# Kernel optimization log

Measured on AMD Instinct MI355X. Metric: run time of the kernel, lower is better.

## Reference

```python
import jax, jax.numpy as jnp
import numpy as np

D = 1024   # cfg.hid (downscaled from 8192)
M = 20000  # cfg.mem_c // 2 (downscaled)
B, LQ = 4, 8
PLAST_S = 0.05
IMPORTANCE = 1.0


def mha_shared_kv(q, kv_k, kv_v, Wi, bi, Wo, bo, nheads):
    """torch nn.MultiheadAttention (batch_first) with batch-shared K/V.
    q: [B,Lq,D]; kv_k/kv_v: [Lk,D] shared across batch (avoids the .repeat()
    materialization in the original torch code while computing identical math)."""
    dh = D // nheads
    Wq, Wk, Wv = jnp.split(Wi, 3, axis=0)
    bq, bk, bv = jnp.split(bi, 3)
    qp = (jnp.einsum('bqd,ed->bqe', q, Wq) + bq) * (dh ** -0.5)
    kp = kv_k @ Wk.T + bk              # [Lk,D]
    vp = kv_v @ Wv.T + bv              # [Lk,D]
    qh = qp.reshape(q.shape[0], q.shape[1], nheads, dh)      # [B,Lq,h,dh]
    kh = kp.reshape(kp.shape[0], nheads, dh)                 # [Lk,h,dh]
    vh = vp.reshape(vp.shape[0], nheads, dh)                 # [Lk,h,dh]
    scores = jnp.einsum('bqhd,khd->bhqk', qh, kh)            # [B,h,Lq,Lk]
    attn = jax.nn.softmax(scores, axis=-1)
    ctx = jnp.einsum('bhqk,khd->bqhd', attn, vh)
    ctx = ctx.reshape(q.shape[0], q.shape[1], D)
    return ctx @ Wo.T + bo


def setup_inputs() -> dict:
    key = jax.random.key(0)
    ks = jax.random.split(key, 16)
    s = 0.02
    return {
        'q':    jax.random.normal(ks[0], (B, LQ, D), jnp.float32),
        'data': jax.random.normal(ks[1], (B, D), jnp.float32),
        'ek':   jax.random.normal(ks[2], (M, D), jnp.float32),
        'ev':   jax.random.normal(ks[3], (M, D), jnp.float32),
        'sk':   jax.random.normal(ks[4], (M, D), jnp.float32),
        'sv':   jax.random.normal(ks[5], (M, D), jnp.float32),
        'wm':   jax.random.normal(ks[6], (10, D), jnp.float32),
        'Wi_e': jax.random.normal(ks[7], (3 * D, D), jnp.float32) * s,
        'bi_e': jnp.zeros((3 * D,), jnp.float32),
        'Wo_e': jax.random.normal(ks[8], (D, D), jnp.float32) * s,
        'bo_e': jnp.zeros((D,), jnp.float32),
        'Wi_s': jax.random.normal(ks[9], (3 * D, D), jnp.float32) * s,
        'bi_s': jnp.zeros((3 * D,), jnp.float32),
        'Wo_s': jax.random.normal(ks[10], (D, D), jnp.float32) * s,
        'bo_s': jnp.zeros((D,), jnp.float32),
        'Wi_w': jax.random.normal(ks[11], (3 * D, D), jnp.float32) * s,
        'bi_w': jnp.zeros((3 * D,), jnp.float32),
        'Wo_w': jax.random.normal(ks[12], (D, D), jnp.float32) * s,
        'bo_w': jnp.zeros((D,), jnp.float32),
        'Wrp':  jax.random.normal(ks[13], (D, 3 * D), jnp.float32) * s,
        'brp':  jnp.zeros((D,), jnp.float32),
        'eu':   jnp.zeros((M,), jnp.float32),
    }


def reference(q, data, ek, ev, sk, sv, wm,
              Wi_e, bi_e, Wo_e, bo_e,
              Wi_s, bi_s, Wo_s, bo_s,
              Wi_w, bi_w, Wo_w, bo_w,
              Wrp, brp, eu):
    # ---- NeuroMemory.read ----
    e_r = mha_shared_kv(q, ek, ev, Wi_e, bi_e, Wo_e, bo_e, 16)
    s_r = mha_shared_kv(q, sk, sv, Wi_s, bi_s, Wo_s, bo_s, 16)
    w_r = mha_shared_kv(q, wm, wm, Wi_w, bi_w, Wo_w, bo_w, 8)
    read_out = jnp.concatenate([e_r, s_r, w_r], axis=-1) @ Wrp.T + brp  # [B,Lq,D]

    # ---- NeuroMemory.write (episodic, Hebbian plasticity update) ----
    scores = data @ ek.T                       # [B,M]
    probs = jax.nn.softmax(scores, axis=-1)    # [B,M]
    upd = probs * (PLAST_S * IMPORTANCE)       # [B,M]
    u = upd.mean(axis=0)[:, None]              # [M,1] (batch-mean update strength)
    d = data.mean(axis=0)[None, :]             # [1,D]
    new_ek = ek * (1.0 - u) + d * u            # [M,D]
    new_ev = ev * (1.0 - u) + d * u            # [M,D]
    new_eu = eu * 0.99 + jax.lax.stop_gradient(probs.sum(axis=0))  # [M]
    return (read_out, new_ek, new_ev, new_eu)
```

## Files before the change

kernel.cpp:

```cpp
#include <hip/hip_runtime.h>
#include <hip/hip_fp16.h>
#include <hip/hip_bf16.h>
#include <cstdint>
#include <cstddef>

#define D_HID 1024
#define MEM_M 20000
#define NBATCH 4
#define BL 32
#define NROWS 512
#define SROWS_E 516
#define SROWS_S 512
#define BK 32
#define LDT 40
#define PV_NC 8

typedef __attribute__((ext_vector_type(8))) short short8;
typedef __attribute__((ext_vector_type(4))) float f32x4;
typedef __attribute__((ext_vector_type(16))) float f32x16;
typedef __attribute__((ext_vector_type(4))) unsigned short us4;

__device__ inline ushort f2bf(float f) {
    __hip_bfloat16 b = __float2bfloat16(f);
    return *reinterpret_cast<ushort*>(&b);
}
__device__ inline float h2f(ushort u) {
    __half h; *reinterpret_cast<ushort*>(&h) = u; return __half2float(h);
}

__device__ __forceinline__ void block_sync_lds() {
    asm volatile("s_waitcnt lgkmcnt(0)" ::: "memory");
    __builtin_amdgcn_s_barrier();
}

struct SkDesc  { const float* A; const float* B; int K; int M; };
struct SkDescs { SkDesc d[5]; };
struct RdDesc  { const float* bias; float* dst; int M; int ldc; float alpha; };
struct RdDescs { RdDesc d[5]; };

__device__ __forceinline__ void skinny_body(const SkDesc dd, float* __restrict__ part,
                                            int gk, int k0, int n0, int tid)
{
    __shared__ float As[32][132];
    __shared__ float Bs[64][129];
    const int K = dd.K, M = dd.M;
    {
        const int r = tid >> 3, cbl = (tid & 7) * 16;
        if (r < M) {
            const float* src = dd.A + (size_t)r * K + k0 + cbl;
            #pragma unroll
            for (int i = 0; i < 4; ++i) {
                const float4 v = *(const float4*)(src + i * 4);
                As[r][cbl + i * 4 + 0] = v.x; As[r][cbl + i * 4 + 1] = v.y;
                As[r][cbl + i * 4 + 2] = v.z; As[r][cbl + i * 4 + 3] = v.w;
            }
        } else {
            #pragma unroll
            for (int i = 0; i < 16; ++i) As[r][cbl + i] = 0.f;
        }
    }
    {
        const int r = tid >> 2, cbl = (tid & 3) * 32;
        const float* src = dd.B + (size_t)(n0 + r) * K + k0 + cbl;
        #pragma unroll
        for (int i = 0; i < 8; ++i) {
            const float4 v = *(const float4*)(src + i * 4);
            Bs[r][cbl + i * 4 + 0] = v.x; Bs[r][cbl + i * 4 + 1] = v.y;
            Bs[r][cbl + i * 4 + 2] = v.z; Bs[r][cbl + i * 4 + 3] = v.w;
        }
    }
    __syncthreads();
    const int n = tid & 63, mg = tid >> 6;
    float acc[8];
    #pragma unroll
    for (int i = 0; i < 8; ++i) acc[i] = 0.f;
    #pragma unroll 4
    for (int k = 0; k < 128; k += 4) {
        const float b0 = Bs[n][k + 0], b1 = Bs[n][k + 1];
        const float b2 = Bs[n][k + 2], b3 = Bs[n][k + 3];
        #pragma unroll
        for (int i = 0; i < 8; ++i) {
            const float4 a = *(const float4*)&As[mg * 8 + i][k];
            acc[i] = fmaf(a.x, b0, fmaf(a.y, b1, fmaf(a.z, b2, fmaf(a.w, b3, acc[i]))));
        }
    }
    #pragma unroll
    for (int i = 0; i < 8; ++i)
        part[((size_t)gk * 32 + mg * 8 + i) * 1024 + n0 + n] = acc[i];
}

__global__ __launch_bounds__(256)
void k_skinny(SkDescs ds, float* __restrict__ part)
{
    skinny_body(ds.d[blockIdx.z], part,
                blockIdx.z * gridDim.y + blockIdx.y,
                blockIdx.y * 128, blockIdx.x * 64, threadIdx.x);
}

__global__ __launch_bounds__(256)
void k_head(SkDescs ds, float* __restrict__ part,
            const float* __restrict__ ek, const float* __restrict__ sk,
            ushort* __restrict__ kvb)
{
    const int bx = blockIdx.x;
    const int tid = threadIdx.x;
    if (bx < 640) {
        const int g = bx >> 7;
        const int rem = bx & 127;
        const int kc = rem >> 4;
        const int n0 = (rem & 15) * 64;
        skinny_body(ds.d[g], part, g * 8 + kc, kc * 128, n0, tid);
    } else {
        const size_t nchunks = (size_t)2 * MEM_M * D_HID / 8;
        for (size_t i = (size_t)(bx - 640) * 256 + tid; i < nchunks;
             i += (size_t)1408 * 256) {
            const size_t base = i * 8;
            const float* src = (base < (size_t)MEM_M * D_HID)
                             ? (ek + base) : (sk + base - (size_t)MEM_M * D_HID);
            const float4 v0 = *(const float4*)(src);
            const float4 v1 = *(const float4*)(src + 4);
            alignas(16) ushort o[8];
            o[0] = f2bf(v0.x); o[1] = f2bf(v0.y); o[2] = f2bf(v0.z); o[3] = f2bf(v0.w);
            o[4] = f2bf(v1.x); o[5] = f2bf(v1.y); o[6] = f2bf(v1.z); o[7] = f2bf(v1.w);
            *(short8*)(kvb + base) = *(const short8*)o;
        }
    }
}

__global__ __launch_bounds__(256)
void k_skred(RdDescs ds, const float* __restrict__ part, int nkc)
{
    const int g = blockIdx.y;
    const int m = blockIdx.x;
    const RdDesc dd = ds.d[g];
    if (m >= dd.M) return;
    const int c = threadIdx.x * 4;
    float4 s = make_float4(0.f, 0.f, 0.f, 0.f);
    for (int kc = 0; kc < nkc; ++kc) {
        const float4 v = *(const float4*)&part[((size_t)(g * nkc + kc) * 32 + m) * 1024 + c];
        s.x += v.x; s.y += v.y; s.z += v.z; s.w += v.w;
    }
    const float4 b = *(const float4*)(dd.bias + c);
    float4 o;
    o.x = (s.x + b.x) * dd.alpha; o.y = (s.y + b.y) * dd.alpha;
    o.z = (s.z + b.z) * dd.alpha; o.w = (s.w + b.w) * dd.alpha;
    *(float4*)(dd.dst + (size_t)m * dd.ldc + c) = o;
}

__global__ __launch_bounds__(256)
void mfma_scores(const ushort* __restrict__ A_e, const ushort* __restrict__ ekb,
                 const ushort* __restrict__ A_s, const ushort* __restrict__ skb,
                 __half* __restrict__ S_e, __half* __restrict__ S_s,
                 __half* __restrict__ swr,
                 const float* __restrict__ c0_e, const float* __restrict__ c0_s)
{
    __shared__ ushort As[2][128][LDT];
    __shared__ ushort Bs[2][128][LDT];
    const int tid = threadIdx.x;
    const int i = blockIdx.x + 9 * blockIdx.y;
    const int xcd = i & 7, idx = i >> 3;
    const int wg = (xcd < 5 ? xcd * 177 : 885 + (xcd - 5) * 176) + idx;
    const int mi = wg % 9, nbk = wg / 9;
    const int bank = (mi >= 5);
    const int m0 = (bank ? (mi - 5) : mi) * 128;
    const int n0 = nbk * 128;
    const ushort* __restrict__ A = bank ? A_s : A_e;
    const ushort* __restrict__ B = bank ? skb : ekb;
    const float* __restrict__ c0 = bank ? c0_s : c0_e;
    const int Mreal = bank ? SROWS_S : SROWS_E;

    const int wid = tid >> 6, lane = tid & 63;
    const int wr = (wid >> 1) * 64, wc = (wid & 1) * 64;
    const int l31 = lane & 31, l2 = lane >> 5;

    const int srow = tid >> 1;
    const int ac = (tid & 1) * 16;
    int gbrow = n0 + srow; if (gbrow > MEM_M - 1) gbrow = MEM_M - 1;
    const ushort* Ap = A + (size_t)(m0 + srow) * 1024 + ac;
    const ushort* Bp = B + (size_t)gbrow * 1024 + ac;

    f32x16 acc[2][2];
    #pragma unroll
    for (int fm = 0; fm < 2; ++fm)
        #pragma unroll
        for (int fn = 0; fn < 2; ++fn)
            #pragma unroll
            for (int r = 0; r < 16; ++r) acc[fm][fn][r] = 0.f;

    auto MF = [&](int bu) {
        short8 a[2][2], b[2][2];
        #pragma unroll
        for (int f = 0; f < 2; ++f)
            #pragma unroll
            for (int kh = 0; kh < 2; ++kh) {
                a[f][kh] = *(const short8*)&As[bu][wr + f * 32 + l31][kh * 16 + l2 * 8];
                b[f][kh] = *(const short8*)&Bs[bu][wc + f * 32 + l31][kh * 16 + l2 * 8];
            }
        #pragma unroll
        for (int fm = 0; fm < 2; ++fm)
            #pragma unroll
            for (int fn = 0; fn < 2; ++fn)
                #pragma unroll
                for (int kh = 0; kh < 2; ++kh)
                    acc[fm][fn] = __builtin_amdgcn_mfma_f32_32x32x16_bf16(
                        a[fm][kh], b[fn][kh], acc[fm][fn], 0, 0, 0);
    };

    short8 a00, a01, b00, b01;
    short8 a10, a11, b10, b11;

#define SC_LOAD0(KT) { a00 = *(const short8*)(Ap + (KT)); a01 = *(const short8*)(Ap + (KT) + 8); \
                       b00 = *(const short8*)(Bp + (KT)); b01 = *(const short8*)(Bp + (KT) + 8); }
#define SC_LOAD1(KT) { a10 = *(const short8*)(Ap + (KT)); a11 = *(const short8*)(Ap + (KT) + 8); \
                       b10 = *(const short8*)(Bp + (KT)); b11 = *(const short8*)(Bp + (KT) + 8); }
#define SC_STORE0(BU) { *(short8*)&As[BU][srow][ac] = a00; *(short8*)&As[BU][srow][ac + 8] = a01; \
                        *(short8*)&Bs[BU][srow][ac] = b00; *(short8*)&Bs[BU][srow][ac + 8] = b01; }
#define SC_STORE1(BU) { *(short8*)&As[BU][srow][ac] = a10; *(short8*)&As[BU][srow][ac + 8] = a11; \
                        *(short8*)&Bs[BU][srow][ac] = b10; *(short8*)&Bs[BU][srow][ac + 8] = b11; }

    SC_LOAD0(0);
    SC_LOAD1(32);
    SC_STORE0(0);
    block_sync_lds();
    for (int it = 0; it < 16; ++it) {
        const int kt = it * 64;
        if (it < 15) SC_LOAD0(kt + 64);
        MF(0);
        SC_STORE1(1);
        block_sync_lds();
        if (it < 15) SC_LOAD1(kt + 96);
        MF(1);
        if (it < 15) SC_STORE0(0);
        block_sync_lds();
    }
#undef SC_LOAD0
#undef SC_LOAD1
#undef SC_STORE0
#undef SC_STORE1

    #pragma unroll
    for (int fm = 0; fm < 2; ++fm) {
        #pragma unroll
        for (int fn = 0; fn < 2; ++fn) {
            #pragma unroll
            for (int r = 0; r < 16; ++r) {
                const int row = m0 + wr + fm * 32 + (r & 3) + 8 * (r >> 2) + 4 * l2;
                if (row >= Mreal) continue;
                const int col = n0 + wc + fn * 32 + l31;
                if (col >= MEM_M) continue;
                const __half hv = __float2half(acc[fm][fn][r] + c0[row]);
                if (bank) S_s[(size_t)row * MEM_M + col] = hv;
                else if (row < NROWS) S_e[(size_t)row * MEM_M + col] = hv;
                else swr[(size_t)(row - NROWS) * MEM_M + col] = hv;
            }
        }
    }
}

__global__ __launch_bounds__(256)
void mfma_pv(const ushort* __restrict__ P_e, const ushort* __restrict__ P_s,
             const ushort* __restrict__ evb, const ushort* __restrict__ svb,
             float* __restrict__ part)
{
    __shared__ ushort As[2][128][LDT];
    __shared__ ushort Bs[2][128][LDT];
    const int tid = threadIdx.x;
    const int bid = blockIdx.x + 8 * (blockIdx.y + 4 * blockIdx.z);
    const int wgs = (bid & 7) * 64 + (bid >> 3);
    const int nI = wgs & 7, mI = (wgs >> 3) & 3;
    const int z = wgs >> 5;
    const int bank = z >> 3, c = z & 7;
    const ushort* __restrict__ P = bank ? P_s : P_e;
    const ushort* __restrict__ Vb = bank ? svb : evb;
    const int m0 = mI * 128, n0 = nI * 128;
    const int ks0 = (c * 625) / PV_NC, ks1 = ((c + 1) * 625) / PV_NC;
    const int wid = tid >> 6, lane = tid & 63;
    const int wr = (wid >> 1) * 64, wc = (wid & 1) * 64;
    const int l31 = lane & 31, l2 = lane >> 5;
    const int kb = (tid & 7) * 4, nb2 = (tid >> 3) * 4;
    const int srow = tid >> 1, ac = (tid & 1) * 16;
    const ushort* Pp = P + (size_t)(m0 + srow) * MEM_M + ac;

    f32x16 acc[2][2];
    #pragma unroll
    for (int fm = 0; fm < 2; ++fm)
        #pragma unroll
        for (int fn = 0; fn < 2; ++fn)
            #pragma unroll
            for (int r = 0; r < 16; ++r) acc[fm][fn][r] = 0.f;

    auto MF = [&](int bu) {
        short8 a[2][2], b[2][2];
        #pragma unroll
        for (int f = 0; f < 2; ++f)
            #pragma unroll
            for (int kh = 0; kh < 2; ++kh) {
                a[f][kh] = *(const short8*)&As[bu][wr + f * 32 + l31][kh * 16 + l2 * 8];
                b[f][kh] = *(const short8*)&Bs[bu][wc + f * 32 + l31][kh * 16 + l2 * 8];
            }
        #pragma unroll
        for (int fm = 0; fm < 2; ++fm)
            #pragma unroll
            for (int fn = 0; fn < 2; ++fn)
                #pragma unroll
                for (int kh = 0; kh < 2; ++kh)
                    acc[fm][fn] = __builtin_amdgcn_mfma_f32_32x32x16_bf16(
                        a[fm][kh], b[fn][kh], acc[fm][fn], 0, 0, 0);
    };

    short8 pa00, pa01, pa10, pa11;
    us4 q0[4], q1[4];

#define PV_LOAD0(T) { const int kt = (T) * 32; \
    pa00 = *(const short8*)(Pp + kt); pa01 = *(const short8*)(Pp + kt + 8); \
    q0[0] = *(const us4*)(Vb + (size_t)(kt + kb + 0) * 1024 + n0 + nb2); \
    q0[1] = *(const us4*)(Vb + (size_t)(kt + kb + 1) * 1024 + n0 + nb2); \
    q0[2] = *(const us4*)(Vb + (size_t)(kt + kb + 2) * 1024 + n0 + nb2); \
    q0[3] = *(const us4*)(Vb + (size_t)(kt + kb + 3) * 1024 + n0 + nb2); }
#define PV_LOAD1(T) { const int kt = (T) * 32; \
    pa10 = *(const short8*)(Pp + kt); pa11 = *(const short8*)(Pp + kt + 8); \
    q1[0] = *(const us4*)(Vb + (size_t)(kt + kb + 0) * 1024 + n0 + nb2); \
    q1[1] = *(const us4*)(Vb + (size_t)(kt + kb + 1) * 1024 + n0 + nb2); \
    q1[2] = *(const us4*)(Vb + (size_t)(kt + kb + 2) * 1024 + n0 + nb2); \
    q1[3] = *(const us4*)(Vb + (size_t)(kt + kb + 3) * 1024 + n0 + nb2); }
#define PV_STORE0(BU) { \
    *(short8*)&As[BU][srow][ac] = pa00; *(short8*)&As[BU][srow][ac + 8] = pa01; \
    us4 w; \
    w.x = q0[0].x; w.y = q0[1].x; w.z = q0[2].x; w.w = q0[3].x; \
    *(us4*)&Bs[BU][nb2 + 0][kb] = w; \
    w.x = q0[0].y; w.y = q0[1].y; w.z = q0[2].y; w.w = q0[3].y; \
    *(us4*)&Bs[BU][nb2 + 1][kb] = w; \
    w.x = q0[0].z; w.y = q0[1].z; w.z = q0[2].z; w.w = q0[3].z; \
    *(us4*)&Bs[BU][nb2 + 2][kb] = w; \
    w.x = q0[0].w; w.y = q0[1].w; w.z = q0[2].w; w.w = q0[3].w; \
    *(us4*)&Bs[BU][nb2 + 3][kb] = w; }
#define PV_STORE1(BU) { \
    *(short8*)&As[BU][srow][ac] = pa10; *(short8*)&As[BU][srow][ac + 8] = pa11; \
    us4 w; \
    w.x = q1[0].x; w.y = q1[1].x; w.z = q1[2].x; w.w = q1[3].x; \
    *(us4*)&Bs[BU][nb2 + 0][kb] = w; \
    w.x = q1[0].y; w.y = q1[1].y; w.z = q1[2].y; w.w = q1[3].y; \
    *(us4*)&Bs[BU][nb2 + 1][kb] = w; \
    w.x = q1[0].z; w.y = q1[1].z; w.z = q1[2].z; w.w = q1[3].z; \
    *(us4*)&Bs[BU][nb2 + 2][kb] = w; \
    w.x = q1[0].w; w.y = q1[1].w; w.z = q1[2].w; w.w = q1[3].w; \
    *(us4*)&Bs[BU][nb2 + 3][kb] = w; }

    PV_LOAD0(ks0);
    if (ks0 + 1 < ks1) PV_LOAD1(ks0 + 1);
    PV_STORE0(0);
    block_sync_lds();
    for (int t = ks0; t < ks1; t += 2) {
        if (t + 2 < ks1) PV_LOAD0(t + 2);
        MF(0);
        if (t + 1 < ks1) PV_STORE1(1);
        block_sync_lds();
        if (t + 1 < ks1) {
            if (t + 3 < ks1) PV_LOAD1(t + 3);
            MF(1);
            if (t + 2 < ks1) PV_STORE0(0);
            block_sync_lds();
        }
    }
#undef PV_LOAD0
#undef PV_LOAD1
#undef PV_STORE0
#undef PV_STORE1

    float* __restrict__ po = part + (size_t)z * NROWS * 1024;
    #pragma unroll
    for (int fm = 0; fm < 2; ++fm)
        #pragma unroll
        for (int fn = 0; fn < 2; ++fn)
            #pragma unroll
            for (int r = 0; r < 16; ++r) {
                const int row = m0 + wr + fm * 32 + (r & 3) + 8 * (r >> 2) + 4 * l2;
                const int col = n0 + wc + fn * 32 + l31;
                po[(size_t)row * 1024 + col] = acc[fm][fn][r];
            }
}

__global__ __launch_bounds__(256)
void k_T(const float* __restrict__ qp,
         const float* __restrict__ Wi_e, const float* __restrict__ bi_e,
         const float* __restrict__ Wi_s, const float* __restrict__ bi_s,
         ushort* __restrict__ A_e, float* __restrict__ c0_e,
         ushort* __restrict__ A_s, float* __restrict__ c0_s,
         const float* __restrict__ data, float* __restrict__ dmean)
{
    const int bq = blockIdx.x;
    const int tid = threadIdx.x;
    if (bq >= 128) {
        if (bq < 252) {
            const int row = SROWS_E + (bq - 128);
            us4 z4; z4.x = 0; z4.y = 0; z4.z = 0; z4.w = 0;
            *(us4*)(A_e + (size_t)row * 1024 + tid * 4) = z4;
        } else {
            for (int t = tid; t < D_HID; t += 256) {
                float s = 0.f;
                #pragma unroll
                for (int b = 0; b < NBATCH; ++b) s += data[b * D_HID + t];
                dmean[t] = 0.25f * s;
                #pragma unroll
                for (int b = 0; b < NBATCH; ++b)
                    A_e[(size_t)(NROWS + b) * 1024 + t] = f2bf(data[b * D_HID + t]);
            }
            if (tid < NBATCH) c0_e[NROWS + tid] = 0.f;
        }
        return;
    }
    const int bank = bq >> 6;
    const int h = (bq >> 2) & 15;
    const int q4 = bq & 3;
    const float* qpB = qp + (size_t)bank * BL * D_HID;
    const float* Wk = (bank ? Wi_s : Wi_e) + (size_t)D_HID * D_HID;
    const float* bk = (bank ? bi_s : bi_e) + D_HID;
    ushort* T  = bank ? A_s : A_e;
    float* c0 = bank ? c0_s : c0_e;

    __shared__ float qs[32][64];
    for (int i = tid; i < 32 * 64; i += 256) {
        const int r = i >> 6, j = i & 63;
        qs[r][j] = qpB[(size_t)r * D_HID + h * 64 + j];
    }
    __syncthreads();
    const int e = q4 * 256 + tid;
    float acc[32];
    #pragma unroll
    for (int r = 0; r < 32; ++r) acc[r] = 0.f;
    for (int j = 0; j < 64; ++j) {
        const float w = Wk[(size_t)(h * 64 + j) * D_HID + e];
        #pragma unroll
        for (int r = 0; r < 32; ++r) acc[r] = fmaf(qs[r][j], w, acc[r]);
    }
    #pragma unroll
    for (int r = 0; r < 32; ++r) T[(size_t)(r * 16 + h) * 1024 + e] = f2bf(acc[r]);
    if (q4 == 0 && tid < 32) {
        float s = 0.f;
        for (int j = 0; j < 64; ++j) s += qs[tid][j] * bk[h * 64 + j];
        c0[tid * 16 + h] = s;
    }
}

__global__ __launch_bounds__(256)
void k_softmax(__half* __restrict__ S_e, __half* __restrict__ S_s,
               __half* __restrict__ swr,
               float* __restrict__ mrow, float* __restrict__ lrow,
               const float* __restrict__ ev, const float* __restrict__ sv,
               ushort* __restrict__ evb, ushort* __restrict__ svb)
{
    const int bx = blockIdx.x;
    const int tid = threadIdx.x;
    if (bx >= SROWS_E + SROWS_S) {
        const size_t nchunks = (size_t)2 * MEM_M * D_HID / 8;
        for (size_t i = (size_t)(bx - (SROWS_E + SROWS_S)) * 256 + tid; i < nchunks;
             i += (size_t)1408 * 256) {
            const size_t base = i * 8;
            const bool second = base >= (size_t)MEM_M * D_HID;
            const float* src = second ? (sv + base - (size_t)MEM_M * D_HID) : (ev + base);
            ushort* dst = second ? (svb + base - (size_t)MEM_M * D_HID) : (evb + base);
            const float4 v0 = *(const float4*)(src);
            const float4 v1 = *(const float4*)(src + 4);
            alignas(16) ushort o[8];
            o[0] = f2bf(v0.x); o[1] = f2bf(v0.y); o[2] = f2bf(v0.z); o[3] = f2bf(v0.w);
            o[4] = f2bf(v1.x); o[5] = f2bf(v1.y); o[6] = f2bf(v1.z); o[7] = f2bf(v1.w);
            *(short8*)dst = *(const short8*)o;
        }
        return;
    }
    const int row = bx;
    ushort* p; bool conv = true;
    if (row < NROWS) p = (ushort*)(S_e + (size_t)row * MEM_M);
    else if (row < SROWS_E) { p = (ushort*)(swr + (size_t)(row - NROWS) * MEM_M); conv = false; }
    else p = (ushort*)(S_s + (size_t)(row - SROWS_E) * MEM_M);
    __shared__ float red_m[256];
    __shared__ float red_l[256];
    float m = -3.0e38f, l = 0.f;
    for (int c = tid; c < MEM_M / 8; c += 256) {
        alignas(16) ushort t[8];
        *(short8*)t = *(const short8*)(p + c * 8);
        float v[8];
        #pragma unroll
        for (int j = 0; j < 8; ++j) v[j] = h2f(t[j]);
        float cm = v[0];
        #pragma unroll
        for (int j = 1; j < 8; ++j) cm = fmaxf(cm, v[j]);
        const float nm = fmaxf(m, cm);
        float s = 0.f;
        #pragma unroll
        for (int j = 0; j < 8; ++j) s += __expf(v[j] - nm);
        l = l * __expf(m - nm) + s;
        m = nm;
    }
    red_m[tid] = m; red_l[tid] = l; __syncthreads();
    for (int s = 128; s > 0; s >>= 1) {
        if (tid < s) {
            const float m2 = fmaxf(red_m[tid], red_m[tid + s]);
            red_l[tid] = red_l[tid] * __expf(red_m[tid] - m2)
                       + red_l[tid + s] * __expf(red_m[tid + s] - m2);
            red_m[tid] = m2;
        }
        __syncthreads();
    }
    const float rm = red_m[0];
    if (conv) {
        for (int c = tid; c < MEM_M / 8; c += 256) {
            alignas(16) ushort t[8];
            *(short8*)t = *(const short8*)(p + c * 8);
            alignas(16) ushort o[8];
            #pragma unroll
            for (int j = 0; j < 8; ++j) o[j] = f2bf(__expf(h2f(t[j]) - rm));
            *(short8*)(p + c * 8) = *(const short8*)o;
        }
    }
    if (tid == 0) { mrow[row] = rm; lrow[row] = red_l[0]; }
}

__global__ __launch_bounds__(256)
void k_uk(const __half* __restrict__ swr,
          const float* __restrict__ mrow, const float* __restrict__ lrow,
          const float* __restrict__ eu,
          float* __restrict__ u, float* __restrict__ out_eu)
{
    const int k = blockIdx.x * 256 + threadIdx.x;
    if (k >= MEM_M) return;
    float sp = 0.f;
    #pragma unroll
    for (int b = 0; b < NBATCH; ++b) {
        const int row = NROWS + b;
        sp += __expf(__half2float(swr[(size_t)b * MEM_M + k]) - mrow[row]) / lrow[row];
    }
    u[k] = 0.05f * 0.25f * sp;
    out_eu[k] = eu[k] * 0.99f + sp;
}

__global__ __launch_bounds__(256)
void k_pvred_upd(const float* __restrict__ part, const float* __restrict__ lrow,
                 float* __restrict__ R,
                 const float* __restrict__ ev, const float* __restrict__ u,
                 const float* __restrict__ dmean, float* __restrict__ out_ev)
{
    const int tid = threadIdx.x;
    if (blockIdx.x < 1024) {
        const size_t perb4 = (size_t)NROWS * 1024 / 4;
        const size_t i = (size_t)blockIdx.x * 256 + tid;
        const int bank = i >= perb4;
        const size_t off4 = i - (size_t)bank * perb4;
        const int m = (int)(off4 >> 8);
        const float inv = 1.f / lrow[bank ? (SROWS_E + m) : m];
        const float4* p = (const float4*)part + (size_t)bank * PV_NC * perb4 + off4;
        float4 s = make_float4(0.f, 0.f, 0.f, 0.f);
        #pragma unroll
        for (int c = 0; c < PV_NC; ++c) {
            const float4 v = p[(size_t)c * perb4];
            s.x += v.x; s.y += v.y; s.z += v.z; s.w += v.w;
        }
        s.x *= inv; s.y *= inv; s.z *= inv; s.w *= inv;
        ((float4*)R)[i] = s;
    } else {
        const int bid = blockIdx.x - 1024;
        const size_t n4 = (size_t)MEM_M * D_HID / 4;
        for (size_t i = (size_t)bid * 256 + tid; i < n4; i += (size_t)1024 * 256) {
            const int k = (int)(i >> 8);
            const int c = (int)(i & 255);
            const float uk = u[k];
            const float om = 1.f - uk;
            const float4 dd = ((const float4*)dmean)[c];
            const float4 b = ((const float4*)ev)[i];
            float4 ob;
            ob.x = b.x * om + dd.x * uk; ob.y = b.y * om + dd.y * uk;
            ob.z = b.z * om + dd.z * uk; ob.w = b.w * om + dd.w * uk;
            ((float4*)out_ev)[i] = ob;
        }
    }
}

__global__ __launch_bounds__(256)
void k_tail(const float* __restrict__ R,
            const float* __restrict__ Wi_e, const float* __restrict__ bi_e,
            const float* __restrict__ Wi_s, const float* __restrict__ bi_s,
            float* __restrict__ ctx,
            const float* __restrict__ qp, const float* __restrict__ kpw,
            const float* __restrict__ vpw,
            const float* __restrict__ ek, const float* __restrict__ u,
            const float* __restrict__ dmean, float* __restrict__ out_ek)
{
    __shared__ float sm[12384];
    const int tid = threadIdx.x;
    const int bx = blockIdx.x;
    if (bx < 32) {
        const int bank = bx >> 4;
        const int h = bx & 15;
        const float* Rb = R + (size_t)bank * NROWS * D_HID;
        const float* Wv = (bank ? Wi_s : Wi_e) + (size_t)2 * D_HID * D_HID;
        const float* bv = (bank ? bi_s : bi_e) + 2 * D_HID;
        float* cb = ctx + (size_t)bank * BL * D_HID;
        float (*Rs)[129] = (float(*)[129])sm;
        float (*Ws)[129] = (float(*)[129])(sm + 32 * 129);
        const int j = tid & 63;
        const int g = tid >> 6;
        float acc[8];
        #pragma unroll
        for (int i = 0; i < 8; ++i) acc[i] = 0.f;
        for (int ec = 0; ec < D_HID; ec += 128) {
            for (int i = tid; i < 32 * 128; i += 256) {
                const int r = i >> 7, e = i & 127;
                Rs[r][e] = Rb[(size_t)(r * 16 + h) * D_HID + ec + e];
            }
            for (int i = tid; i < 64 * 128; i += 256) {
                const int r = i >> 7, e = i & 127;
                Ws[r][e] = Wv[(size_t)(h * 64 + r) * D_HID + ec + e];
            }
            __syncthreads();
            for (int e = 0; e < 128; ++e) {
                const float w = Ws[j][e];
                #pragma unroll
                for (int i = 0; i < 8; ++i)
                    acc[i] = fmaf(Rs[g + 4 * i][e], w, acc[i]);
            }
            __syncthreads();
        }
        #pragma unroll
        for (int i = 0; i < 8; ++i) {
            const int bl = g + 4 * i;
            cb[(size_t)bl * D_HID + h * 64 + j] = acc[i] + bv[h * 64 + j];
        }
    } else if (bx < 64) {
        const int bl = bx - 32;
        float* q = sm;
        float (*kp)[1024] = (float(*)[1024])(sm + 1024);
        float (*pp)[10] = (float(*)[10])(sm + 1024 + 10240);
        const float* qrow = qp + (size_t)(2 * BL + bl) * D_HID;
        for (int i = tid; i < D_HID; i += 256) q[i] = qrow[i];
        for (int i = tid; i < 10 * D_HID; i += 256) kp[i >> 10][i & 1023] = kpw[i];
        __syncthreads();
        if (tid < 80) {
            const int h = tid / 10, k = tid % 10;
            float s = 0.f;
            for (int jj = 0; jj < 128; ++jj) s += q[h * 128 + jj] * kp[k][h * 128 + jj];
            pp[h][k] = s;
        }
        __syncthreads();
        if (tid < 8) {
            float m = -3.0e38f;
            for (int k = 0; k < 10; ++k) m = fmaxf(m, pp[tid][k]);
            float e[10]; float l = 0.f;
            for (int k = 0; k < 10; ++k) { e[k] = __expf(pp[tid][k] - m); l += e[k]; }
            const float inv = 1.f / l;
            for (int k = 0; k < 10; ++k) pp[tid][k] = e[k] * inv;
        }
        __syncthreads();
        float* cw = ctx + (size_t)(2 * BL + bl) * D_HID;
        for (int f = tid; f < D_HID; f += 256) {
            const int h = f >> 7;
            float s = 0.f;
            #pragma unroll
            for (int k = 0; k < 10; ++k) s += pp[h][k] * vpw[(size_t)k * D_HID + f];
            cw[f] = s;
        }
    } else {
        const int bid = bx - 64;
        const size_t n4 = (size_t)MEM_M * D_HID / 4;
        for (size_t i = (size_t)bid * 256 + tid; i < n4; i += (size_t)1024 * 256) {
            const int k = (int)(i >> 8);
            const int c = (int)(i & 255);
            const float uk = u[k];
            const float om = 1.f - uk;
            const float4 dd = ((const float4*)dmean)[c];
            const float4 a = ((const float4*)ek)[i];
            float4 oa;
            oa.x = a.x * om + dd.x * uk; oa.y = a.y * om + dd.y * uk;
            oa.z = a.z * om + dd.z * uk; oa.w = a.w * om + dd.w * uk;
            ((float4*)out_ek)[i] = oa;
        }
    }
}

extern "C" void kernel_launch(void* const* d_in, const int* in_sizes, int n_in,
                              void* d_out, int out_size, void* d_ws, size_t ws_size,
                              hipStream_t stream)
{
    (void)in_sizes; (void)n_in; (void)out_size; (void)ws_size;
    const float* q    = (const float*)d_in[0];
    const float* data = (const float*)d_in[1];
    const float* ek   = (const float*)d_in[2];
    const float* ev   = (const float*)d_in[3];
    const float* sk   = (const float*)d_in[4];
    const float* sv   = (const float*)d_in[5];
    const float* wm   = (const float*)d_in[6];
    const float* Wi_e = (const float*)d_in[7];
    const float* bi_e = (const float*)d_in[8];
    const float* Wo_e = (const float*)d_in[9];
    const float* bo_e = (const float*)d_in[10];
    const float* Wi_s = (const float*)d_in[11];
    const float* bi_s = (const float*)d_in[12];
    const float* Wo_s = (const float*)d_in[13];
    const float* bo_s = (const float*)d_in[14];
    const float* Wi_w = (const float*)d_in[15];
    const float* bi_w = (const float*)d_in[16];
    const float* Wo_w = (const float*)d_in[17];
    const float* bo_w = (const float*)d_in[18];
    const float* Wrp  = (const float*)d_in[19];
    const float* brp  = (const float*)d_in[20];
    const float* eu   = (const float*)d_in[21];

    float* out = (float*)d_out;
    float* out_read = out;
    float* out_ek = out + 32768;
    float* out_ev = out_ek + 20480000;
    float* out_eu = out_ev + 20480000;

    float* ws    = (float*)d_ws;
    float* qp    = ws;
    float* A_e   = qp + 98304;
    float* A_s   = A_e + 655360;
    float* c0_e  = A_s + 524288;
    float* c0_s  = c0_e + 640;
    float* dmean = c0_s + 512;
    float* u     = dmean + 1024;
    float* mrow  = u + 20480;
    float* lrow  = mrow + 1032;
    float* kpw   = lrow + 1032;
    float* vpw   = kpw + 10240;
    float* ctx   = vpw + 10240;
    float* cat   = ctx + 98304;
    float* skpart = cat + 98304;
    float* Rbuf  = skpart;
    __half* swr  = (__half*)(skpart + 1310720);

    ushort* A_e16 = (ushort*)A_e;
    ushort* A_s16 = (ushort*)A_s;

    ushort* ekb = (ushort*)out_ek;
    ushort* skb = ekb + (size_t)MEM_M * D_HID;
    ushort* evb = (ushort*)out_ek;
    float* part = out_ek + 10240000;
    __half* S_e = (__half*)out_ev;
    __half* S_s = S_e + (size_t)NROWS * MEM_M;
    ushort* svb = (ushort*)(S_s + (size_t)NROWS * MEM_M);

    const dim3 b256(256);
    const float sc16 = 0.125f;
    const float sc8  = 0.08838834764831845f;

    SkDescs s1;
    s1.d[0] = {q,  Wi_e,            1024, 32};
    s1.d[1] = {q,  Wi_s,            1024, 32};
    s1.d[2] = {q,  Wi_w,            1024, 32};
    s1.d[3] = {wm, Wi_w + 1048576,  1024, 10};
    s1.d[4] = {wm, Wi_w + 2097152,  1024, 10};
    k_head<<<2048, b256, 0, stream>>>(s1, skpart, ek, sk, ekb);
    RdDescs r1;
    r1.d[0] = {bi_e,        qp,         32, 1024, sc16};
    r1.d[1] = {bi_s,        qp + 32768, 32, 1024, sc16};
    r1.d[2] = {bi_w,        qp + 65536, 32, 1024, sc8};
    r1.d[3] = {bi_w + 1024, kpw,        10, 1024, 1.f};
    r1.d[4] = {bi_w + 2048, vpw,        10, 1024, 1.f};
    k_skred<<<dim3(32, 5), b256, 0, stream>>>(r1, skpart, 8);

    k_T<<<253, b256, 0, stream>>>(qp, Wi_e, bi_e, Wi_s, bi_s,
                                  A_e16, c0_e, A_s16, c0_s, data, dmean);

    mfma_scores<<<dim3(9, 157), b256, 0, stream>>>(A_e16, ekb, A_s16, skb,
                                                   S_e, S_s, swr, c0_e, c0_s);

    k_softmax<<<SROWS_E + SROWS_S + 1408, b256, 0, stream>>>(
        S_e, S_s, swr, mrow, lrow, ev, sv, evb, svb);
    k_uk<<<79, b256, 0, stream>>>(swr, mrow, lrow, eu, u, out_eu);

    mfma_pv<<<dim3(8, 4, 2 * PV_NC), b256, 0, stream>>>(
        (const ushort*)S_e, (const ushort*)S_s, evb, svb, part);

    k_pvred_upd<<<2048, b256, 0, stream>>>(part, lrow, Rbuf, ev, u, dmean, out_ev);

    k_tail<<<1088, b256, 0, stream>>>(Rbuf, Wi_e, bi_e, Wi_s, bi_s, ctx,
                                      qp, kpw, vpw, ek, u, dmean, out_ek);

    SkDescs s2;
    s2.d[0] = {ctx,         Wo_e, 1024, 32};
    s2.d[1] = {ctx + 32768, Wo_s, 1024, 32};
    s2.d[2] = {ctx + 65536, Wo_w, 1024, 32};
    s2.d[3] = {ctx,         Wo_e, 1024, 32};
    s2.d[4] = {ctx,         Wo_e, 1024, 32};
    k_skinny<<<dim3(16, 8, 3), b256, 0, stream>>>(s2, skpart);
    RdDescs r2;
    r2.d[0] = {bo_e, cat,        32, 3072, 1.f};
    r2.d[1] = {bo_s, cat + 1024, 32, 3072, 1.f};
    r2.d[2] = {bo_w, cat + 2048, 32, 3072, 1.f};
    r2.d[3] = r2.d[0];
    r2.d[4] = r2.d[0];
    k_skred<<<dim3(32, 3), b256, 0, stream>>>(r2, skpart, 8);

    SkDescs s3;
    s3.d[0] = {cat, Wrp, 3072, 32};
    s3.d[1] = s3.d[0]; s3.d[2] = s3.d[0]; s3.d[3] = s3.d[0]; s3.d[4] = s3.d[0];
    k_skinny<<<dim3(16, 24, 1), b256, 0, stream>>>(s3, skpart);
    RdDescs r3;
    r3.d[0] = {brp, out_read, 32, 1024, 1.f};
    r3.d[1] = r3.d[0]; r3.d[2] = r3.d[0]; r3.d[3] = r3.d[0]; r3.d[4] = r3.d[0];
    k_skred<<<dim3(32, 1), b256, 0, stream>>>(r3, skpart, 24);
}
```

Baseline: 497.8 us.

## Fuse exp and row-sum into score GEMM epilogue, drop max-subtraction softmax pass

The score GEMM epilogue now writes exp(score) as bf16 straight into the P buffers and accumulates per-row sums with a warp shuffle reduction plus atomicAdd. This removes the separate softmax kernel that re-read and rewrote the full fp16 score matrices. Only the four write-path rows still get a small max/sum stats kernel, and the ev/sv bf16 conversion moves into k_uk. The trade-off is that the row max is no longer subtracted, so numerical safety rests on scores being small enough not to overflow exp. Row-sum atomics also make the summation order nondeterministic.

```diff
diff --git a/kernel.cpp b/kernel.cpp
--- a/kernel.cpp
+++ b/kernel.cpp
@@ -150,9 +150,10 @@
 __global__ __launch_bounds__(256)
 void mfma_scores(const ushort* __restrict__ A_e, const ushort* __restrict__ ekb,
                  const ushort* __restrict__ A_s, const ushort* __restrict__ skb,
-                 __half* __restrict__ S_e, __half* __restrict__ S_s,
+                 ushort* __restrict__ P_e, ushort* __restrict__ P_s,
                  __half* __restrict__ swr,
-                 const float* __restrict__ c0_e, const float* __restrict__ c0_s)
+                 const float* __restrict__ c0_e, const float* __restrict__ c0_s,
+                 float* __restrict__ lrow)
 {
     __shared__ ushort As[2][128][LDT];
     __shared__ ushort Bs[2][128][LDT];
@@ -166,6 +167,7 @@
     const int n0 = nbk * 128;
     const ushort* __restrict__ A = bank ? A_s : A_e;
     const ushort* __restrict__ B = bank ? skb : ekb;
+    ushort* __restrict__ P = bank ? P_s : P_e;
     const float* __restrict__ c0 = bank ? c0_s : c0_e;
     const int Mreal = bank ? SROWS_S : SROWS_E;
 
@@ -241,17 +243,31 @@
     #pragma unroll
     for (int fm = 0; fm < 2; ++fm) {
         #pragma unroll
-        for (int fn = 0; fn < 2; ++fn) {
-            #pragma unroll
-            for (int r = 0; r < 16; ++r) {
-                const int row = m0 + wr + fm * 32 + (r & 3) + 8 * (r >> 2) + 4 * l2;
-                if (row >= Mreal) continue;
+        for (int rr = 0; rr < 16; ++rr) {
+            const int row = m0 + wr + fm * 32 + (rr & 3) + 8 * (rr >> 2) + 4 * l2;
+            if (row >= Mreal) continue;
+            const bool wpath = (!bank) && (row >= NROWS);
+            const float cr = c0[row];
+            float lsum = 0.f;
+            #pragma unroll
+            for (int fn = 0; fn < 2; ++fn) {
                 const int col = n0 + wc + fn * 32 + l31;
                 if (col >= MEM_M) continue;
-                const __half hv = __float2half(acc[fm][fn][r] + c0[row]);
-                if (bank) S_s[(size_t)row * MEM_M + col] = hv;
-                else if (row < NROWS) S_e[(size_t)row * MEM_M + col] = hv;
-                else swr[(size_t)(row - NROWS) * MEM_M + col] = hv;
+                const float sv_ = acc[fm][fn][rr] + cr;
+                if (wpath) {
+                    swr[(size_t)(row - NROWS) * MEM_M + col] = __float2half(sv_);
+                } else {
+                    const float e = __expf(sv_);
+                    P[(size_t)row * MEM_M + col] = f2bf(e);
+                    lsum += e;
+                }
+            }
+            if (!wpath) {
+                #pragma unroll
+                for (int off = 1; off < 32; off <<= 1)
+                    lsum += __shfl_xor(lsum, off);
+                if (l31 == 0)
+                    atomicAdd(&lrow[bank ? (SROWS_E + row) : row], lsum);
             }
         }
     }
@@ -386,7 +402,8 @@
          const float* __restrict__ Wi_s, const float* __restrict__ bi_s,
          ushort* __restrict__ A_e, float* __restrict__ c0_e,
          ushort* __restrict__ A_s, float* __restrict__ c0_s,
-         const float* __restrict__ data, float* __restrict__ dmean)
+         const float* __restrict__ data, float* __restrict__ dmean,
+         float* __restrict__ lrow)
 {
     const int bq = blockIdx.x;
     const int tid = threadIdx.x;
@@ -406,6 +423,7 @@
                     A_e[(size_t)(NROWS + b) * 1024 + t] = f2bf(data[b * D_HID + t]);
             }
             if (tid < NBATCH) c0_e[NROWS + tid] = 0.f;
+            for (int t = tid; t < SROWS_E + SROWS_S; t += 256) lrow[t] = 0.f;
         }
         return;
     }
@@ -443,17 +461,57 @@
 }
 
 __global__ __launch_bounds__(256)
-void k_softmax(__half* __restrict__ S_e, __half* __restrict__ S_s,
-               __half* __restrict__ swr,
-               float* __restrict__ mrow, float* __restrict__ lrow,
-               const float* __restrict__ ev, const float* __restrict__ sv,
-               ushort* __restrict__ evb, ushort* __restrict__ svb)
+void k_wstat(const __half* __restrict__ swr,
+             float* __restrict__ mrow, float* __restrict__ lrow)
+{
+    const int b = blockIdx.x;
+    const ushort* p = (const ushort*)swr + (size_t)b * MEM_M;
+    __shared__ float red_m[256];
+    __shared__ float red_l[256];
+    const int tid = threadIdx.x;
+    float m = -3.0e38f, l = 0.f;
+    for (int c = tid; c < MEM_M / 8; c += 256) {
+        alignas(16) ushort t[8];
+        *(short8*)t = *(const short8*)(p + c * 8);
+        float v[8];
+        #pragma unroll
+        for (int j = 0; j < 8; ++j) v[j] = h2f(t[j]);
+        float cm = v[0];
+        #pragma unroll
+        for (int j = 1; j < 8; ++j) cm = fmaxf(cm, v[j]);
+        const float nm = fmaxf(m, cm);
+        float s = 0.f;
+        #pragma unroll
+        for (int j = 0; j < 8; ++j) s += __expf(v[j] - nm);
+        l = l * __expf(m - nm) + s;
+        m = nm;
+    }
+    red_m[tid] = m; red_l[tid] = l; __syncthreads();
+    for (int s = 128; s > 0; s >>= 1) {
+        if (tid < s) {
+            const float m2 = fmaxf(red_m[tid], red_m[tid + s]);
+            red_l[tid] = red_l[tid] * __expf(red_m[tid] - m2)
+                       + red_l[tid + s] * __expf(red_m[tid + s] - m2);
+            red_m[tid] = m2;
+        }
+        __syncthreads();
+    }
+    if (tid == 0) { mrow[NROWS + b] = red_m[0]; lrow[NROWS + b] = red_l[0]; }
+}
+
+__global__ __launch_bounds__(256)
+void k_uk(const __half* __restrict__ swr,
+          const float* __restrict__ mrow, const float* __restrict__ lrow,
+          const float* __restrict__ eu,
+          float* __restrict__ u, float* __restrict__ out_eu,
+          const float* __restrict__ ev, const float* __restrict__ sv,
+          ushort* __restrict__ evb, ushort* __restrict__ svb)
 {
     const int bx = blockIdx.x;
     const int tid = threadIdx.x;
-    if (bx >= SROWS_E + SROWS_S) {
+    if (bx >= 79) {
         const size_t nchunks = (size_t)2 * MEM_M * D_HID / 8;
-        for (size_t i = (size_t)(bx - (SROWS_E + SROWS_S)) * 256 + tid; i < nchunks;
+        for (size_t i = (size_t)(bx - 79) * 256 + tid; i < nchunks;
              i += (size_t)1408 * 256) {
             const size_t base = i * 8;
             const bool second = base >= (size_t)MEM_M * D_HID;
@@ -468,61 +526,7 @@
         }
         return;
     }
-    const int row = bx;
-    ushort* p; bool conv = true;
-    if (row < NROWS) p = (ushort*)(S_e + (size_t)row * MEM_M);
-    else if (row < SROWS_E) { p = (ushort*)(swr + (size_t)(row - NROWS) * MEM_M); conv = false; }
-    else p = (ushort*)(S_s + (size_t)(row - SROWS_E) * MEM_M);
-    __shared__ float red_m[256];
-    __shared__ float red_l[256];
-    float m = -3.0e38f, l = 0.f;
-    for (int c = tid; c < MEM_M / 8; c += 256) {
-        alignas(16) ushort t[8];
-        *(short8*)t = *(const short8*)(p + c * 8);
-        float v[8];
-        #pragma unroll
-        for (int j = 0; j < 8; ++j) v[j] = h2f(t[j]);
-        float cm = v[0];
-        #pragma unroll
-        for (int j = 1; j < 8; ++j) cm = fmaxf(cm, v[j]);
-        const float nm = fmaxf(m, cm);
-        float s = 0.f;
-        #pragma unroll
-        for (int j = 0; j < 8; ++j) s += __expf(v[j] - nm);
-        l = l * __expf(m - nm) + s;
-        m = nm;
-    }
-    red_m[tid] = m; red_l[tid] = l; __syncthreads();
-    for (int s = 128; s > 0; s >>= 1) {
-        if (tid < s) {
-            const float m2 = fmaxf(red_m[tid], red_m[tid + s]);
-            red_l[tid] = red_l[tid] * __expf(red_m[tid] - m2)
-                       + red_l[tid + s] * __expf(red_m[tid + s] - m2);
-            red_m[tid] = m2;
-        }
-        __syncthreads();
-    }
-    const float rm = red_m[0];
-    if (conv) {
-        for (int c = tid; c < MEM_M / 8; c += 256) {
-            alignas(16) ushort t[8];
-            *(short8*)t = *(const short8*)(p + c * 8);
-            alignas(16) ushort o[8];
-            #pragma unroll
-            for (int j = 0; j < 8; ++j) o[j] = f2bf(__expf(h2f(t[j]) - rm));
-            *(short8*)(p + c * 8) = *(const short8*)o;
-        }
-    }
-    if (tid == 0) { mrow[row] = rm; lrow[row] = red_l[0]; }
-}
-
-__global__ __launch_bounds__(256)
-void k_uk(const __half* __restrict__ swr,
-          const float* __restrict__ mrow, const float* __restrict__ lrow,
-          const float* __restrict__ eu,
-          float* __restrict__ u, float* __restrict__ out_eu)
-{
-    const int k = blockIdx.x * 256 + threadIdx.x;
+    const int k = bx * 256 + tid;
     if (k >= MEM_M) return;
     float sp = 0.f;
     #pragma unroll
@@ -735,9 +739,9 @@
     ushort* skb = ekb + (size_t)MEM_M * D_HID;
     ushort* evb = (ushort*)out_ek;
     float* part = out_ek + 10240000;
-    __half* S_e = (__half*)out_ev;
-    __half* S_s = S_e + (size_t)NROWS * MEM_M;
-    ushort* svb = (ushort*)(S_s + (size_t)NROWS * MEM_M);
+    ushort* P_e = (ushort*)out_ev;
+    ushort* P_s = P_e + (size_t)NROWS * MEM_M;
+    ushort* svb = P_s + (size_t)NROWS * MEM_M;
 
     const dim3 b256(256);
     const float sc16 = 0.125f;
@@ -759,17 +763,16 @@
     k_skred<<<dim3(32, 5), b256, 0, stream>>>(r1, skpart, 8);
 
     k_T<<<253, b256, 0, stream>>>(qp, Wi_e, bi_e, Wi_s, bi_s,
-                                  A_e16, c0_e, A_s16, c0_s, data, dmean);
+                                  A_e16, c0_e, A_s16, c0_s, data, dmean, lrow);
 
     mfma_scores<<<dim3(9, 157), b256, 0, stream>>>(A_e16, ekb, A_s16, skb,
-                                                   S_e, S_s, swr, c0_e, c0_s);
-
-    k_softmax<<<SROWS_E + SROWS_S + 1408, b256, 0, stream>>>(
-        S_e, S_s, swr, mrow, lrow, ev, sv, evb, svb);
-    k_uk<<<79, b256, 0, stream>>>(swr, mrow, lrow, eu, u, out_eu);
-
-    mfma_pv<<<dim3(8, 4, 2 * PV_NC), b256, 0, stream>>>(
-        (const ushort*)S_e, (const ushort*)S_s, evb, svb, part);
+                                                   P_e, P_s, swr, c0_e, c0_s, lrow);
+
+    k_wstat<<<4, b256, 0, stream>>>(swr, mrow, lrow);
+    k_uk<<<79 + 1408, b256, 0, stream>>>(swr, mrow, lrow, eu, u, out_eu,
+                                         ev, sv, evb, svb);
+
+    mfma_pv<<<dim3(8, 4, 2 * PV_NC), b256, 0, stream>>>(P_e, P_s, evb, svb, part);
 
     k_pvred_upd<<<2048, b256, 0, stream>>>(part, lrow, Rbuf, ev, u, dmean, out_ev);
 
```

Result: slower. 564.9 us (+13.5%).
